# Kernel optimization log

Hardware: AMD Instinct MI355X
Metric: run time of the kernel (lower is better)

The kernel has to match this reference:

```python
import jax, jax.numpy as jnp
import numpy as np

NUM_HEADS = 8

def setup_inputs() -> dict:
    key = jax.random.key(0)
    ks = jax.random.split(key, 12)
    T, B, C, D = 2048, 4, 512, 512
    s = 1.0 / np.sqrt(C)
    return {
        "key_in": jax.random.normal(ks[0], (T, B, C), jnp.float32),
        "value_in": jax.random.normal(ks[1], (T, B, C), jnp.float32),
        "query_in": jax.random.normal(ks[2], (T, B, C), jnp.float32),
        "Wk": jax.random.normal(ks[3], (C, D), jnp.float32) * s,
        "bk": jax.random.normal(ks[4], (D,), jnp.float32) * 0.01,
        "Wv": jax.random.normal(ks[5], (C, D), jnp.float32) * s,
        "bv": jax.random.normal(ks[6], (D,), jnp.float32) * 0.01,
        "Wq": jax.random.normal(ks[7], (C, D), jnp.float32) * s,
        "bq": jax.random.normal(ks[8], (D,), jnp.float32) * 0.01,
        "Wo": jax.random.normal(ks[9], (D, D), jnp.float32) * (1.0 / np.sqrt(D)),
        "bo": jax.random.normal(ks[10], (D,), jnp.float32) * 0.01,
    }

def reference(key_in, value_in, query_in, Wk, bk, Wv, bv, Wq, bq, Wo, bo):
    T, B, C = query_in.shape
    D = Wq.shape[1]
    H = NUM_HEADS
    hd = D // H
    scale = 1.0 / np.sqrt(hd).astype(np.float32)
    # Linear projections on (T, B, C) -> (T, B, D), then the original's
    # row-major view(B, -1, H, hd) followed by transpose(1, 2) -> (B, H, T, hd)
    def proj(x, W, b):
        y = x @ W + b                      # (T, B, D)
        return y.reshape(B, -1, H, hd).transpose(0, 2, 1, 3)  # (B, H, T, hd)
    q = proj(query_in, Wq, bq)
    k = proj(key_in, Wk, bk)
    v = proj(value_in, Wv, bv)
    scores = jnp.einsum("bhqd,bhkd->bhqk", q, k) * scale  # (B, H, T, T)
    attn = jax.nn.softmax(scores, axis=-1)
    x = jnp.einsum("bhqk,bhkd->bhqd", attn, v)            # (B, H, T, hd)
    x = x.transpose(0, 2, 1, 3).reshape(T, B, D)          # matches .view(T, B, d_model)
    return x @ Wo + bo
```

## Files before the change

### kernel.cpp

```cpp
#include <hip/hip_runtime.h>
#include <math.h>

#define MROWS 8192
#define DM    512
#define SEQL  2048
#define HDIM  64
#define NSPLIT 2

typedef __attribute__((ext_vector_type(4))) float floatx4;
typedef _Float16 half2v __attribute__((ext_vector_type(2)));
typedef _Float16 half4v __attribute__((ext_vector_type(4)));
typedef _Float16 half8v __attribute__((ext_vector_type(8)));

#define CEXP 0.18033688011f

__device__ __forceinline__ void gll16(const void* g, void* l) {
    __builtin_amdgcn_global_load_lds(
        (const __attribute__((address_space(1))) unsigned int*)g,
        (__attribute__((address_space(3))) unsigned int*)l, 16, 0, 0);
}

__device__ __forceinline__ half4v pack4(float a, float b, float c, float d) {
    half2v lo = __builtin_bit_cast(half2v, __builtin_amdgcn_cvt_pkrtz(a, b));
    half2v hi = __builtin_bit_cast(half2v, __builtin_amdgcn_cvt_pkrtz(c, d));
    half4v r;
    r[0] = lo[0]; r[1] = lo[1]; r[2] = hi[0]; r[3] = hi[1];
    return r;
}

__global__ __launch_bounds__(256) void transw(const float* __restrict__ w0,
                                              const float* __restrict__ w1,
                                              const float* __restrict__ w2,
                                              const float* __restrict__ w3,
                                              _Float16* __restrict__ t0,
                                              _Float16* __restrict__ t1,
                                              _Float16* __restrict__ t2,
                                              _Float16* __restrict__ t3) {
    __shared__ float tile[32][33];
    const float* W = blockIdx.z == 0 ? w0 : (blockIdx.z == 1 ? w1 : (blockIdx.z == 2 ? w2 : w3));
    _Float16* T = blockIdx.z == 0 ? t0 : (blockIdx.z == 1 ? t1 : (blockIdx.z == 2 ? t2 : t3));
    const float sc = (blockIdx.z == 0) ? CEXP : 1.0f;
    const int tx = threadIdx.x & 31, ty = threadIdx.x >> 5;
    const int x = blockIdx.x * 32 + tx;
    const int y0 = blockIdx.y * 32;
#pragma unroll
    for (int i = 0; i < 4; ++i)
        tile[ty + i * 8][tx] = W[(size_t)(y0 + ty + i * 8) * DM + x];
    __syncthreads();
    const int xo = y0 + tx;
#pragma unroll
    for (int i = 0; i < 4; ++i)
        T[(size_t)(blockIdx.x * 32 + ty + i * 8) * DM + xo] = (_Float16)(tile[tx][ty + i * 8] * sc);
}

__global__ __launch_bounds__(256, 3) void proj_gemm(
        const float* __restrict__ q32, const float* __restrict__ k32, const float* __restrict__ v32,
        const _Float16* __restrict__ Wq, const _Float16* __restrict__ Wk, const _Float16* __restrict__ Wv,
        const float* __restrict__ bq, const float* __restrict__ bk, const float* __restrict__ bv,
        _Float16* __restrict__ Qo, _Float16* __restrict__ Ko, _Float16* __restrict__ Vto) {
    __shared__ _Float16 Bs[512 * 32];
    __shared__ _Float16 As[32 * 32];
    const int z = blockIdx.y;
    const float* A32    = z == 0 ? q32 : (z == 1 ? k32 : v32);
    const _Float16* Bt  = z == 0 ? Wq : (z == 1 ? Wk : Wv);
    const float* bias   = z == 0 ? bq : (z == 1 ? bk : bv);
    const float bscale  = z == 0 ? CEXP : 1.0f;

    const int tid = threadIdx.x;
    const int w = tid >> 6;
    const int l15 = tid & 15, quad = (tid & 63) >> 4;
    const int m0 = blockIdx.x * 32;

    floatx4 acc[2][8];
#pragma unroll
    for (int i = 0; i < 2; ++i)
#pragma unroll
        for (int j = 0; j < 8; ++j) acc[i][j] = (floatx4){0.f, 0.f, 0.f, 0.f};

    for (int kt = 0; kt < DM / 32; ++kt) {
        __syncthreads();
#pragma unroll
        for (int i = 0; i < 8; ++i) {
            const int c = i * 256 + tid;
            const int row = c >> 2, g = c & 3;
            const int kg = g ^ (row & 3);
            gll16(&Bt[(size_t)row * DM + kt * 32 + kg * 8], &Bs[c * 8]);
        }
        if (tid < 128) {
            const int c = tid;
            const int row = c >> 2, g = c & 3;
            const int kg = g ^ (row & 3);
            const float* src = &A32[(size_t)(m0 + row) * DM + kt * 32 + kg * 8];
            const float4 f0 = *(const float4*)&src[0];
            const float4 f1 = *(const float4*)&src[4];
            half8v o;
            o[0] = (_Float16)f0.x; o[1] = (_Float16)f0.y; o[2] = (_Float16)f0.z; o[3] = (_Float16)f0.w;
            o[4] = (_Float16)f1.x; o[5] = (_Float16)f1.y; o[6] = (_Float16)f1.z; o[7] = (_Float16)f1.w;
            *(half8v*)&As[c * 8] = o;
        }
        __syncthreads();
        half8v af[2], bfr[8];
#pragma unroll
        for (int i = 0; i < 2; ++i) {
            const int row = i * 16 + l15;
            af[i] = *(const half8v*)&As[row * 32 + (quad ^ (row & 3)) * 8];
        }
#pragma unroll
        for (int j = 0; j < 8; ++j) {
            const int row = w * 128 + j * 16 + l15;
            bfr[j] = *(const half8v*)&Bs[row * 32 + (quad ^ (row & 3)) * 8];
        }
#pragma unroll
        for (int i = 0; i < 2; ++i)
#pragma unroll
            for (int j = 0; j < 8; ++j)
                acc[i][j] = __builtin_amdgcn_mfma_f32_16x16x32_f16(af[i], bfr[j], acc[i][j], 0, 0, 0);
    }
#pragma unroll
    for (int j = 0; j < 8; ++j) {
        const int col = w * 128 + j * 16 + l15;
        const float bv4 = bias[col] * bscale;
#pragma unroll
        for (int i = 0; i < 2; ++i) {
            const int rb = m0 + i * 16 + quad * 4;
            if (z == 2) {
                const int g = rb >> 11, seq = rb & 2047;
                half4v pv;
#pragma unroll
                for (int r = 0; r < 4; ++r) pv[r] = (_Float16)(acc[i][j][r] + bv4);
                *(half4v*)&Vto[((size_t)g * DM + col) * SEQL + seq] = pv;
            } else {
                _Float16* oh = z == 0 ? Qo : Ko;
#pragma unroll
                for (int r = 0; r < 4; ++r)
                    oh[(size_t)(rb + r) * DM + col] = (_Float16)(acc[i][j][r] + bv4);
            }
        }
    }
}

__global__ __launch_bounds__(256, 4) void out_gemm(
        const _Float16* __restrict__ Op0, const _Float16* __restrict__ Op1,
        const float* __restrict__ lp,
        const _Float16* __restrict__ Wo, const float* __restrict__ bo,
        float* __restrict__ out) {
    __shared__ _Float16 Bs[256 * 64];
    __shared__ _Float16 As[32 * 64];
    const int tid = threadIdx.x;
    const int w = tid >> 6;
    const int l15 = tid & 15, quad = (tid & 63) >> 4;
    const int n0 = blockIdx.x * 256, m0 = blockIdx.y * 32;

    floatx4 acc[2][4];
#pragma unroll
    for (int i = 0; i < 2; ++i)
#pragma unroll
        for (int j = 0; j < 4; ++j) acc[i][j] = (floatx4){0.f, 0.f, 0.f, 0.f};

    for (int kt = 0; kt < DM / 64; ++kt) {
        __syncthreads();
#pragma unroll
        for (int i = 0; i < 8; ++i) {
            const int c = i * 256 + tid;
            const int row = c >> 3, g = c & 7;
            const int kg = g ^ (row & 7);
            gll16(&Wo[(size_t)(n0 + row) * DM + kt * 64 + kg * 8], &Bs[c * 8]);
        }
        {
            const int c = tid;
            const int row = c >> 3, g = c & 7;
            const int kg = g ^ (row & 7);
            const int grow = m0 + row;
            const size_t off = (size_t)grow * DM + kt * 64 + kg * 8;
            const half8v a = *(const half8v*)&Op0[off];
            const half8v b = *(const half8v*)&Op1[off];
            const float inv = 1.0f / (lp[(size_t)grow * 8 + kt] +
                                      lp[((size_t)MROWS + grow) * 8 + kt]);
            half8v s;
#pragma unroll
            for (int e = 0; e < 8; ++e)
                s[e] = (_Float16)(((float)a[e] + (float)b[e]) * inv);
            *(half8v*)&As[c * 8] = s;
        }
        __syncthreads();
#pragma unroll
        for (int ks = 0; ks < 2; ++ks) {
            half8v af[2], bfr[4];
#pragma unroll
            for (int i = 0; i < 2; ++i) {
                const int row = i * 16 + l15;
                af[i] = *(const half8v*)&As[row * 64 + ((ks * 4 + quad) ^ (row & 7)) * 8];
            }
#pragma unroll
            for (int j = 0; j < 4; ++j) {
                const int row = w * 64 + j * 16 + l15;
                bfr[j] = *(const half8v*)&Bs[row * 64 + ((ks * 4 + quad) ^ (row & 7)) * 8];
            }
#pragma unroll
            for (int i = 0; i < 2; ++i)
#pragma unroll
                for (int j = 0; j < 4; ++j)
                    acc[i][j] = __builtin_amdgcn_mfma_f32_16x16x32_f16(af[i], bfr[j], acc[i][j], 0, 0, 0);
        }
    }
#pragma unroll
    for (int j = 0; j < 4; ++j) {
        const int col = n0 + w * 64 + j * 16 + l15;
        const float bv4 = bo[col];
#pragma unroll
        for (int i = 0; i < 2; ++i) {
            const int rb = m0 + i * 16 + quad * 4;
#pragma unroll
            for (int r = 0; r < 4; ++r)
                out[(size_t)(rb + r) * DM + col] = acc[i][j][r] + bv4;
        }
    }
}

__global__ __launch_bounds__(256, 4) void attn_mfma(const _Float16* __restrict__ Q16,
                                                    const _Float16* __restrict__ K16,
                                                    const _Float16* __restrict__ Vt,
                                                    _Float16* __restrict__ Opart,
                                                    float* __restrict__ lpart) {
    __shared__ _Float16 Ks[2][64 * 64];
    __shared__ _Float16 Vs[2][64 * 64];

    const int tid  = threadIdx.x;
    const int lane = tid & 63;
    const int l15  = lane & 15;
    const int quad = lane >> 4;

    const int pair  = blockIdx.y;
    const int split = blockIdx.z;
    const int grp   = pair >> 3;
    const int h     = pair & 7;
    const int q0    = blockIdx.x * 128;
    const int rQ    = grp * SEQL + q0 + (tid >> 6) * 32;
    const int cb    = h * HDIM;
    const int NIT   = (SEQL / 64) / NSPLIT;
    const int kt0   = split * NIT;

    const _Float16* Kbase = K16 + (size_t)grp * SEQL * DM + cb;
    const _Float16* Vbase = Vt + (size_t)grp * DM * SEQL + (size_t)cb * SEQL;

    half8v qf[2][2];
#pragma unroll
    for (int qt = 0; qt < 2; ++qt)
#pragma unroll
        for (int ks = 0; ks < 2; ++ks)
            qf[qt][ks] = *(const half8v*)&Q16[(size_t)(rQ + qt * 16 + l15) * DM + cb + ks * 32 + quad * 8];

    floatx4 oacc[2][4], lacc[2];
#pragma unroll
    for (int qt = 0; qt < 2; ++qt) {
        lacc[qt] = (floatx4){0.f, 0.f, 0.f, 0.f};
#pragma unroll
        for (int dt = 0; dt < 4; ++dt) oacc[qt][dt] = (floatx4){0.f, 0.f, 0.f, 0.f};
    }
    half4v ones;
    ones[0] = (_Float16)1.f; ones[1] = (_Float16)1.f; ones[2] = (_Float16)1.f; ones[3] = (_Float16)1.f;

#define STAGE(KT, B)                                                            \
    {                                                                           \
        _Float16* ksb = &Ks[B][0];                                              \
        _Float16* vsb = &Vs[B][0];                                              \
        _Pragma("unroll")                                                       \
        for (int i_ = 0; i_ < 4; ++i_) {                                        \
            const int c_ = i_ * 256 + tid;                                      \
            if (c_ < 512) {                                                     \
                const int key_ = c_ >> 3, g_ = c_ & 7;                          \
                const int dg_ = g_ ^ (key_ & 7);                                \
                gll16(&Kbase[(size_t)((KT) * 64 + key_) * DM + dg_ * 8],        \
                      &ksb[c_ * 8]);                                            \
            } else {                                                            \
                const int cv_ = c_ - 512;                                       \
                const int d_ = cv_ >> 3, g_ = cv_ & 7;                          \
                const int kg_ = g_ ^ (d_ & 7);                                  \
                gll16(&Vbase[(size_t)d_ * SEQL + (KT) * 64 + kg_ * 8],          \
                      &vsb[cv_ * 8]);                                           \
            }                                                                   \
        }                                                                       \
    }

    STAGE(kt0, 0)

    for (int it = 0; it < NIT; ++it) {
        const int cur = it & 1;
        __syncthreads();
        if (it + 1 < NIT) STAGE(kt0 + it + 1, cur ^ 1)

        const _Float16* ksb = &Ks[cur][0];
        const _Float16* vsb = &Vs[cur][0];

        floatx4 st[4][2];
#pragma unroll
        for (int ktile = 0; ktile < 4; ++ktile) {
            const int key = ktile * 16 + l15;
            const half8v kf0 = *(const half8v*)&ksb[key * 64 + ((0 + quad) ^ (key & 7)) * 8];
            const half8v kf1 = *(const half8v*)&ksb[key * 64 + ((4 + quad) ^ (key & 7)) * 8];
#pragma unroll
            for (int qt = 0; qt < 2; ++qt) {
                floatx4 z = {0.f, 0.f, 0.f, 0.f};
                z = __builtin_amdgcn_mfma_f32_16x16x32_f16(kf0, qf[qt][0], z, 0, 0, 0);
                st[ktile][qt] = __builtin_amdgcn_mfma_f32_16x16x32_f16(kf1, qf[qt][1], z, 0, 0, 0);
            }
        }

        half4v pa[4][2];
#pragma unroll
        for (int ktile = 0; ktile < 4; ++ktile)
#pragma unroll
            for (int qt = 0; qt < 2; ++qt)
                pa[ktile][qt] = pack4(__builtin_amdgcn_exp2f(st[ktile][qt][0]),
                                      __builtin_amdgcn_exp2f(st[ktile][qt][1]),
                                      __builtin_amdgcn_exp2f(st[ktile][qt][2]),
                                      __builtin_amdgcn_exp2f(st[ktile][qt][3]));

#pragma unroll
        for (int qt = 0; qt < 2; ++qt)
#pragma unroll
            for (int ktile = 0; ktile < 4; ++ktile)
                lacc[qt] = __builtin_amdgcn_mfma_f32_16x16x16f16(pa[ktile][qt], ones, lacc[qt], 0, 0, 0);

#pragma unroll
        for (int dt = 0; dt < 4; ++dt) {
            const int d = dt * 16 + l15;
#pragma unroll
            for (int ktile = 0; ktile < 4; ++ktile) {
                const int G = ktile * 2 + (quad >> 1);
                const int slot = G ^ (d & 7);
                const half4v vf = *(const half4v*)&vsb[d * 64 + slot * 8 + (quad & 1) * 4];
#pragma unroll
                for (int qt = 0; qt < 2; ++qt)
                    oacc[qt][dt] = __builtin_amdgcn_mfma_f32_16x16x16f16(pa[ktile][qt], vf, oacc[qt][dt], 0, 0, 0);
            }
        }
    }

    _Float16* Op = Opart + (size_t)split * MROWS * DM;
#pragma unroll
    for (int qt = 0; qt < 2; ++qt)
#pragma unroll
        for (int r = 0; r < 4; ++r) {
            const int qrow = rQ + qt * 16 + quad * 4 + r;
            const size_t rowoff = (size_t)qrow * DM + cb;
#pragma unroll
            for (int dt = 0; dt < 4; ++dt)
                Op[rowoff + dt * 16 + l15] = (_Float16)oacc[qt][dt][r];
            if (l15 == 0)
                lpart[((size_t)split * MROWS + qrow) * 8 + h] = lacc[qt][r];
        }
}

extern "C" void kernel_launch(void* const* d_in, const int* in_sizes, int n_in,
                              void* d_out, int out_size, void* d_ws, size_t ws_size,
                              hipStream_t stream) {
    const float* key_in   = (const float*)d_in[0];
    const float* value_in = (const float*)d_in[1];
    const float* query_in = (const float*)d_in[2];
    const float* Wk = (const float*)d_in[3];
    const float* bk = (const float*)d_in[4];
    const float* Wv = (const float*)d_in[5];
    const float* bv = (const float*)d_in[6];
    const float* Wq = (const float*)d_in[7];
    const float* bq = (const float*)d_in[8];
    const float* Wo = (const float*)d_in[9];
    const float* bo = (const float*)d_in[10];
    float* out = (float*)d_out;

    const size_t MAT = (size_t)MROWS * DM;
    _Float16* Q16  = (_Float16*)d_ws;
    _Float16* K16  = Q16 + MAT;
    _Float16* Vtb  = K16 + MAT;
    _Float16* Wqt  = Vtb + MAT;
    _Float16* Wkt  = Wqt + DM * DM;
    _Float16* Wvt  = Wkt + DM * DM;
    _Float16* Wot  = Wvt + DM * DM;
    float*    lpart = (float*)(Wot + DM * DM);
    _Float16* Opart = (_Float16*)(lpart + 2 * MROWS * 8);

    const dim3 blk(256);

    transw<<<dim3(16, 16, 4), blk, 0, stream>>>(Wq, Wk, Wv, Wo, Wqt, Wkt, Wvt, Wot);

    proj_gemm<<<dim3(MROWS / 32, 3), blk, 0, stream>>>(
        query_in, key_in, value_in, Wqt, Wkt, Wvt, bq, bk, bv, Q16, K16, Vtb);

    attn_mfma<<<dim3(SEQL / 128, 32, NSPLIT), blk, 0, stream>>>(Q16, K16, Vtb, Opart, lpart);

    out_gemm<<<dim3(2, MROWS / 32), blk, 0, stream>>>(
        Opart, Opart + MAT, lpart, Wot, bo, out);
}
```

Measured before the change: 201.6 us.

## Fuse four MHA kernels into one persistent cooperative kernel with grid syncs

The weight transpose, QKV projection, attention and output GEMM are folded into one persistent cooperative kernel. Phases are separated by grid.sync and each block loops over work units, with shared memory reused across phases. This aims to remove per-launch overhead and the gaps between kernels. The output GEMM tile also shrinks to 128 columns, giving more work units. In exchange, grid-wide barriers are added, occupancy is capped at the largest shared-memory footprint of any phase, and blocks may sit idle when a phase's work does not divide evenly across the grid. If the cooperative launch fails, the code falls back to four separate kernel launches.

New measurement: 458.1 us. 2.27x slower.

```diff
diff --git a/kernel.cpp b/kernel.cpp
--- a/kernel.cpp
+++ b/kernel.cpp
@@ -1,5 +1,8 @@
 #include <hip/hip_runtime.h>
+#include <hip/hip_cooperative_groups.h>
 #include <math.h>
+
+namespace cg = cooperative_groups;
 
 #define MROWS 8192
 #define DM    512
@@ -13,6 +16,18 @@
 typedef _Float16 half8v __attribute__((ext_vector_type(8)));
 
 #define CEXP 0.18033688011f
+
+#define SMEM_BYTES 34816
+
+struct MhaArgs {
+    const float *q32, *k32, *v32;
+    const float *Wq32, *Wk32, *Wv32, *Wo32;
+    const float *bq, *bk, *bv, *bo;
+    _Float16 *Wqt, *Wkt, *Wvt, *Wot;
+    _Float16 *Q16, *K16, *Vtb, *Opart;
+    float *lpart;
+    float *out;
+};
 
 __device__ __forceinline__ void gll16(const void* g, void* l) {
     __builtin_amdgcn_global_load_lds(
@@ -28,48 +43,40 @@
     return r;
 }
 
-__global__ __launch_bounds__(256) void transw(const float* __restrict__ w0,
-                                              const float* __restrict__ w1,
-                                              const float* __restrict__ w2,
-                                              const float* __restrict__ w3,
-                                              _Float16* __restrict__ t0,
-                                              _Float16* __restrict__ t1,
-                                              _Float16* __restrict__ t2,
-                                              _Float16* __restrict__ t3) {
-    __shared__ float tile[32][33];
-    const float* W = blockIdx.z == 0 ? w0 : (blockIdx.z == 1 ? w1 : (blockIdx.z == 2 ? w2 : w3));
-    _Float16* T = blockIdx.z == 0 ? t0 : (blockIdx.z == 1 ? t1 : (blockIdx.z == 2 ? t2 : t3));
-    const float sc = (blockIdx.z == 0) ? CEXP : 1.0f;
-    const int tx = threadIdx.x & 31, ty = threadIdx.x >> 5;
-    const int x = blockIdx.x * 32 + tx;
-    const int y0 = blockIdx.y * 32;
+__device__ __forceinline__ void phase0(const MhaArgs& a, int u, int tid,
+                                       unsigned char* smem) {
+    float* tile = (float*)smem;
+    const int z = u >> 8, t = u & 255;
+    const float* W = z == 0 ? a.Wq32 : (z == 1 ? a.Wk32 : (z == 2 ? a.Wv32 : a.Wo32));
+    _Float16* T = z == 0 ? a.Wqt : (z == 1 ? a.Wkt : (z == 2 ? a.Wvt : a.Wot));
+    const float sc = (z == 0) ? CEXP : 1.0f;
+    const int tx = tid & 31, ty = tid >> 5;
+    const int x = (t & 15) * 32 + tx;
+    const int y0 = (t >> 4) * 32;
+    __syncthreads();
 #pragma unroll
     for (int i = 0; i < 4; ++i)
-        tile[ty + i * 8][tx] = W[(size_t)(y0 + ty + i * 8) * DM + x];
+        tile[(ty + i * 8) * 33 + tx] = W[(size_t)(y0 + ty + i * 8) * DM + x];
     __syncthreads();
     const int xo = y0 + tx;
 #pragma unroll
     for (int i = 0; i < 4; ++i)
-        T[(size_t)(blockIdx.x * 32 + ty + i * 8) * DM + xo] = (_Float16)(tile[tx][ty + i * 8] * sc);
-}
-
-__global__ __launch_bounds__(256, 3) void proj_gemm(
-        const float* __restrict__ q32, const float* __restrict__ k32, const float* __restrict__ v32,
-        const _Float16* __restrict__ Wq, const _Float16* __restrict__ Wk, const _Float16* __restrict__ Wv,
-        const float* __restrict__ bq, const float* __restrict__ bk, const float* __restrict__ bv,
-        _Float16* __restrict__ Qo, _Float16* __restrict__ Ko, _Float16* __restrict__ Vto) {
-    __shared__ _Float16 Bs[512 * 32];
-    __shared__ _Float16 As[32 * 32];
-    const int z = blockIdx.y;
-    const float* A32    = z == 0 ? q32 : (z == 1 ? k32 : v32);
-    const _Float16* Bt  = z == 0 ? Wq : (z == 1 ? Wk : Wv);
-    const float* bias   = z == 0 ? bq : (z == 1 ? bk : bv);
-    const float bscale  = z == 0 ? CEXP : 1.0f;
-
-    const int tid = threadIdx.x;
+        T[(size_t)((t & 15) * 32 + ty + i * 8) * DM + xo] =
+            (_Float16)(tile[tx * 33 + ty + i * 8] * sc);
+}
+
+__device__ __forceinline__ void phase1(const MhaArgs& a, int u, int tid,
+                                       unsigned char* smem) {
+    _Float16* Bs = (_Float16*)smem;
+    _Float16* As = (_Float16*)(smem + 32768);
     const int w = tid >> 6;
     const int l15 = tid & 15, quad = (tid & 63) >> 4;
-    const int m0 = blockIdx.x * 32;
+    const int z = u >> 8;
+    const int m0 = (u & 255) * 32;
+    const float* A32   = z == 0 ? a.q32 : (z == 1 ? a.k32 : a.v32);
+    const _Float16* Bt = z == 0 ? a.Wqt : (z == 1 ? a.Wkt : a.Wvt);
+    const float* bias  = z == 0 ? a.bq : (z == 1 ? a.bk : a.bv);
+    const float bscale = z == 0 ? CEXP : 1.0f;
 
     floatx4 acc[2][8];
 #pragma unroll
@@ -128,9 +135,9 @@
                 half4v pv;
 #pragma unroll
                 for (int r = 0; r < 4; ++r) pv[r] = (_Float16)(acc[i][j][r] + bv4);
-                *(half4v*)&Vto[((size_t)g * DM + col) * SEQL + seq] = pv;
+                *(half4v*)&a.Vtb[((size_t)g * DM + col) * SEQL + seq] = pv;
             } else {
-                _Float16* oh = z == 0 ? Qo : Ko;
+                _Float16* oh = z == 0 ? a.Q16 : a.K16;
 #pragma unroll
                 for (int r = 0; r < 4; ++r)
                     oh[(size_t)(rb + r) * DM + col] = (_Float16)(acc[i][j][r] + bv4);
@@ -139,116 +146,33 @@
     }
 }
 
-__global__ __launch_bounds__(256, 4) void out_gemm(
-        const _Float16* __restrict__ Op0, const _Float16* __restrict__ Op1,
-        const float* __restrict__ lp,
-        const _Float16* __restrict__ Wo, const float* __restrict__ bo,
-        float* __restrict__ out) {
-    __shared__ _Float16 Bs[256 * 64];
-    __shared__ _Float16 As[32 * 64];
-    const int tid = threadIdx.x;
+__device__ __forceinline__ void phase2(const MhaArgs& a, int u, int tid,
+                                       unsigned char* smem) {
+    _Float16* KsB = (_Float16*)smem;
+    _Float16* VsB = (_Float16*)(smem + 16384);
     const int w = tid >> 6;
     const int l15 = tid & 15, quad = (tid & 63) >> 4;
-    const int n0 = blockIdx.x * 256, m0 = blockIdx.y * 32;
-
-    floatx4 acc[2][4];
-#pragma unroll
-    for (int i = 0; i < 2; ++i)
-#pragma unroll
-        for (int j = 0; j < 4; ++j) acc[i][j] = (floatx4){0.f, 0.f, 0.f, 0.f};
-
-    for (int kt = 0; kt < DM / 64; ++kt) {
-        __syncthreads();
-#pragma unroll
-        for (int i = 0; i < 8; ++i) {
-            const int c = i * 256 + tid;
-            const int row = c >> 3, g = c & 7;
-            const int kg = g ^ (row & 7);
-            gll16(&Wo[(size_t)(n0 + row) * DM + kt * 64 + kg * 8], &Bs[c * 8]);
-        }
-        {
-            const int c = tid;
-            const int row = c >> 3, g = c & 7;
-            const int kg = g ^ (row & 7);
-            const int grow = m0 + row;
-            const size_t off = (size_t)grow * DM + kt * 64 + kg * 8;
-            const half8v a = *(const half8v*)&Op0[off];
-            const half8v b = *(const half8v*)&Op1[off];
-            const float inv = 1.0f / (lp[(size_t)grow * 8 + kt] +
-                                      lp[((size_t)MROWS + grow) * 8 + kt]);
-            half8v s;
-#pragma unroll
-            for (int e = 0; e < 8; ++e)
-                s[e] = (_Float16)(((float)a[e] + (float)b[e]) * inv);
-            *(half8v*)&As[c * 8] = s;
-        }
-        __syncthreads();
-#pragma unroll
-        for (int ks = 0; ks < 2; ++ks) {
-            half8v af[2], bfr[4];
-#pragma unroll
-            for (int i = 0; i < 2; ++i) {
-                const int row = i * 16 + l15;
-                af[i] = *(const half8v*)&As[row * 64 + ((ks * 4 + quad) ^ (row & 7)) * 8];
-            }
-#pragma unroll
-            for (int j = 0; j < 4; ++j) {
-                const int row = w * 64 + j * 16 + l15;
-                bfr[j] = *(const half8v*)&Bs[row * 64 + ((ks * 4 + quad) ^ (row & 7)) * 8];
-            }
-#pragma unroll
-            for (int i = 0; i < 2; ++i)
-#pragma unroll
-                for (int j = 0; j < 4; ++j)
-                    acc[i][j] = __builtin_amdgcn_mfma_f32_16x16x32_f16(af[i], bfr[j], acc[i][j], 0, 0, 0);
-        }
-    }
-#pragma unroll
-    for (int j = 0; j < 4; ++j) {
-        const int col = n0 + w * 64 + j * 16 + l15;
-        const float bv4 = bo[col];
-#pragma unroll
-        for (int i = 0; i < 2; ++i) {
-            const int rb = m0 + i * 16 + quad * 4;
-#pragma unroll
-            for (int r = 0; r < 4; ++r)
-                out[(size_t)(rb + r) * DM + col] = acc[i][j][r] + bv4;
-        }
-    }
-}
-
-__global__ __launch_bounds__(256, 4) void attn_mfma(const _Float16* __restrict__ Q16,
-                                                    const _Float16* __restrict__ K16,
-                                                    const _Float16* __restrict__ Vt,
-                                                    _Float16* __restrict__ Opart,
-                                                    float* __restrict__ lpart) {
-    __shared__ _Float16 Ks[2][64 * 64];
-    __shared__ _Float16 Vs[2][64 * 64];
-
-    const int tid  = threadIdx.x;
-    const int lane = tid & 63;
-    const int l15  = lane & 15;
-    const int quad = lane >> 4;
-
-    const int pair  = blockIdx.y;
-    const int split = blockIdx.z;
+
+    const int qtile = u & 15;
+    const int pair  = (u >> 4) & 31;
+    const int split = u >> 9;
     const int grp   = pair >> 3;
     const int h     = pair & 7;
-    const int q0    = blockIdx.x * 128;
-    const int rQ    = grp * SEQL + q0 + (tid >> 6) * 32;
+    const int q0    = qtile * 128;
+    const int rQ    = grp * SEQL + q0 + w * 32;
     const int cb    = h * HDIM;
     const int NIT   = (SEQL / 64) / NSPLIT;
     const int kt0   = split * NIT;
 
-    const _Float16* Kbase = K16 + (size_t)grp * SEQL * DM + cb;
-    const _Float16* Vbase = Vt + (size_t)grp * DM * SEQL + (size_t)cb * SEQL;
+    const _Float16* Kbase = a.K16 + (size_t)grp * SEQL * DM + cb;
+    const _Float16* Vbase = a.Vtb + (size_t)grp * DM * SEQL + (size_t)cb * SEQL;
 
     half8v qf[2][2];
 #pragma unroll
     for (int qt = 0; qt < 2; ++qt)
 #pragma unroll
         for (int ks = 0; ks < 2; ++ks)
-            qf[qt][ks] = *(const half8v*)&Q16[(size_t)(rQ + qt * 16 + l15) * DM + cb + ks * 32 + quad * 8];
+            qf[qt][ks] = *(const half8v*)&a.Q16[(size_t)(rQ + qt * 16 + l15) * DM + cb + ks * 32 + quad * 8];
 
     floatx4 oacc[2][4], lacc[2];
 #pragma unroll
@@ -262,8 +186,8 @@
 
 #define STAGE(KT, B)                                                            \
     {                                                                           \
-        _Float16* ksb = &Ks[B][0];                                              \
-        _Float16* vsb = &Vs[B][0];                                              \
+        _Float16* ksb = &KsB[(B) * 4096];                                       \
+        _Float16* vsb = &VsB[(B) * 4096];                                       \
         _Pragma("unroll")                                                       \
         for (int i_ = 0; i_ < 4; ++i_) {                                        \
             const int c_ = i_ * 256 + tid;                                      \
@@ -289,8 +213,8 @@
         __syncthreads();
         if (it + 1 < NIT) STAGE(kt0 + it + 1, cur ^ 1)
 
-        const _Float16* ksb = &Ks[cur][0];
-        const _Float16* vsb = &Vs[cur][0];
+        const _Float16* ksb = &KsB[cur * 4096];
+        const _Float16* vsb = &VsB[cur * 4096];
 
         floatx4 st[4][2];
 #pragma unroll
@@ -300,9 +224,9 @@
             const half8v kf1 = *(const half8v*)&ksb[key * 64 + ((4 + quad) ^ (key & 7)) * 8];
 #pragma unroll
             for (int qt = 0; qt < 2; ++qt) {
-                floatx4 z = {0.f, 0.f, 0.f, 0.f};
-                z = __builtin_amdgcn_mfma_f32_16x16x32_f16(kf0, qf[qt][0], z, 0, 0, 0);
-                st[ktile][qt] = __builtin_amdgcn_mfma_f32_16x16x32_f16(kf1, qf[qt][1], z, 0, 0, 0);
+                floatx4 z2 = {0.f, 0.f, 0.f, 0.f};
+                z2 = __builtin_amdgcn_mfma_f32_16x16x32_f16(kf0, qf[qt][0], z2, 0, 0, 0);
+                st[ktile][qt] = __builtin_amdgcn_mfma_f32_16x16x32_f16(kf1, qf[qt][1], z2, 0, 0, 0);
             }
         }
 
@@ -336,8 +260,9 @@
             }
         }
     }
-
-    _Float16* Op = Opart + (size_t)split * MROWS * DM;
+#undef STAGE
+
+    _Float16* Op = a.Opart + (size_t)split * MROWS * DM;
 #pragma unroll
     for (int qt = 0; qt < 2; ++qt)
 #pragma unroll
@@ -348,46 +273,159 @@
             for (int dt = 0; dt < 4; ++dt)
                 Op[rowoff + dt * 16 + l15] = (_Float16)oacc[qt][dt][r];
             if (l15 == 0)
-                lpart[((size_t)split * MROWS + qrow) * 8 + h] = lacc[qt][r];
-        }
+                a.lpart[((size_t)split * MROWS + qrow) * 8 + h] = lacc[qt][r];
+        }
+}
+
+__device__ __forceinline__ void phase3(const MhaArgs& a, int u, int tid,
+                                       unsigned char* smem) {
+    _Float16* Bs = (_Float16*)smem;
+    _Float16* As = (_Float16*)(smem + 16384);
+    const int w = tid >> 6;
+    const int l15 = tid & 15, quad = (tid & 63) >> 4;
+    const int n0 = (u & 3) * 128;
+    const int m0 = (u >> 2) * 32;
+
+    floatx4 acc[2][2];
+#pragma unroll
+    for (int i = 0; i < 2; ++i)
+#pragma unroll
+        for (int j = 0; j < 2; ++j) acc[i][j] = (floatx4){0.f, 0.f, 0.f, 0.f};
+
+    for (int kt = 0; kt < DM / 64; ++kt) {
+        __syncthreads();
+#pragma unroll
+        for (int i = 0; i < 4; ++i) {
+            const int c = i * 256 + tid;
+            const int row = c >> 3, g = c & 7;
+            const int kg = g ^ (row & 7);
+            gll16(&a.Wot[(size_t)(n0 + row) * DM + kt * 64 + kg * 8], &Bs[c * 8]);
+        }
+        {
+            const int c = tid;
+            const int row = c >> 3, g = c & 7;
+            const int kg = g ^ (row & 7);
+            const int grow = m0 + row;
+            const size_t off = (size_t)grow * DM + kt * 64 + kg * 8;
+            const half8v av = *(const half8v*)&a.Opart[off];
+            const half8v bv = *(const half8v*)&a.Opart[(size_t)MROWS * DM + off];
+            const float inv = 1.0f / (a.lpart[(size_t)grow * 8 + kt] +
+                                      a.lpart[((size_t)MROWS + grow) * 8 + kt]);
+            half8v s;
+#pragma unroll
+            for (int e = 0; e < 8; ++e)
+                s[e] = (_Float16)(((float)av[e] + (float)bv[e]) * inv);
+            *(half8v*)&As[c * 8] = s;
+        }
+        __syncthreads();
+#pragma unroll
+        for (int ks = 0; ks < 2; ++ks) {
+            half8v af[2], bfr[2];
+#pragma unroll
+            for (int i = 0; i < 2; ++i) {
+                const int row = i * 16 + l15;
+                af[i] = *(const half8v*)&As[row * 64 + ((ks * 4 + quad) ^ (row & 7)) * 8];
+            }
+#pragma unroll
+            for (int j = 0; j < 2; ++j) {
+                const int row = w * 32 + j * 16 + l15;
+                bfr[j] = *(const half8v*)&Bs[row * 64 + ((ks * 4 + quad) ^ (row & 7)) * 8];
+            }
+#pragma unroll
+            for (int i = 0; i < 2; ++i)
+#pragma unroll
+                for (int j = 0; j < 2; ++j)
+                    acc[i][j] = __builtin_amdgcn_mfma_f32_16x16x32_f16(af[i], bfr[j], acc[i][j], 0, 0, 0);
+        }
+    }
+#pragma unroll
+    for (int j = 0; j < 2; ++j) {
+        const int col = n0 + w * 32 + j * 16 + l15;
+        const float bv4 = a.bo[col];
+#pragma unroll
+        for (int i = 0; i < 2; ++i) {
+            const int rb = m0 + i * 16 + quad * 4;
+#pragma unroll
+            for (int r = 0; r < 4; ++r)
+                a.out[(size_t)(rb + r) * DM + col] = acc[i][j][r] + bv4;
+        }
+    }
+}
+
+__global__ __launch_bounds__(256, 4) void fused_mha(MhaArgs a) {
+    __shared__ __align__(16) unsigned char smem[SMEM_BYTES];
+    cg::grid_group grid = cg::this_grid();
+    const int tid = threadIdx.x;
+    for (unsigned u = blockIdx.x; u < 1024; u += gridDim.x) phase0(a, u, tid, smem);
+    grid.sync();
+    for (unsigned u = blockIdx.x; u < 768; u += gridDim.x) phase1(a, u, tid, smem);
+    grid.sync();
+    for (unsigned u = blockIdx.x; u < 1024; u += gridDim.x) phase2(a, u, tid, smem);
+    grid.sync();
+    for (unsigned u = blockIdx.x; u < 1024; u += gridDim.x) phase3(a, u, tid, smem);
+}
+
+__global__ __launch_bounds__(256, 4) void k_p0(MhaArgs a) {
+    __shared__ __align__(16) unsigned char smem[SMEM_BYTES];
+    phase0(a, blockIdx.x, threadIdx.x, smem);
+}
+__global__ __launch_bounds__(256, 4) void k_p1(MhaArgs a) {
+    __shared__ __align__(16) unsigned char smem[SMEM_BYTES];
+    phase1(a, blockIdx.x, threadIdx.x, smem);
+}
+__global__ __launch_bounds__(256, 4) void k_p2(MhaArgs a) {
+    __shared__ __align__(16) unsigned char smem[SMEM_BYTES];
+    phase2(a, blockIdx.x, threadIdx.x, smem);
+}
+__global__ __launch_bounds__(256, 4) void k_p3(MhaArgs a) {
+    __shared__ __align__(16) unsigned char smem[SMEM_BYTES];
+    phase3(a, blockIdx.x, threadIdx.x, smem);
 }
 
 extern "C" void kernel_launch(void* const* d_in, const int* in_sizes, int n_in,
                               void* d_out, int out_size, void* d_ws, size_t ws_size,
                               hipStream_t stream) {
-    const float* key_in   = (const float*)d_in[0];
-    const float* value_in = (const float*)d_in[1];
-    const float* query_in = (const float*)d_in[2];
-    const float* Wk = (const float*)d_in[3];
-    const float* bk = (const float*)d_in[4];
-    const float* Wv = (const float*)d_in[5];
-    const float* bv = (const float*)d_in[6];
-    const float* Wq = (const float*)d_in[7];
-    const float* bq = (const float*)d_in[8];
-    const float* Wo = (const float*)d_in[9];
-    const float* bo = (const float*)d_in[10];
-    float* out = (float*)d_out;
+    MhaArgs a;
+    a.k32  = (const float*)d_in[0];
+    a.v32  = (const float*)d_in[1];
+    a.q32  = (const float*)d_in[2];
+    a.Wk32 = (const float*)d_in[3];
+    a.bk   = (const float*)d_in[4];
+    a.Wv32 = (const float*)d_in[5];
+    a.bv   = (const float*)d_in[6];
+    a.Wq32 = (const float*)d_in[7];
+    a.bq   = (const float*)d_in[8];
+    a.Wo32 = (const float*)d_in[9];
+    a.bo   = (const float*)d_in[10];
+    a.out  = (float*)d_out;
 
     const size_t MAT = (size_t)MROWS * DM;
-    _Float16* Q16  = (_Float16*)d_ws;
-    _Float16* K16  = Q16 + MAT;
-    _Float16* Vtb  = K16 + MAT;
-    _Float16* Wqt  = Vtb + MAT;
-    _Float16* Wkt  = Wqt + DM * DM;
-    _Float16* Wvt  = Wkt + DM * DM;
-    _Float16* Wot  = Wvt + DM * DM;
-    float*    lpart = (float*)(Wot + DM * DM);
-    _Float16* Opart = (_Float16*)(lpart + 2 * MROWS * 8);
-
-    const dim3 blk(256);
-
-    transw<<<dim3(16, 16, 4), blk, 0, stream>>>(Wq, Wk, Wv, Wo, Wqt, Wkt, Wvt, Wot);
-
-    proj_gemm<<<dim3(MROWS / 32, 3), blk, 0, stream>>>(
-        query_in, key_in, value_in, Wqt, Wkt, Wvt, bq, bk, bv, Q16, K16, Vtb);
-
-    attn_mfma<<<dim3(SEQL / 128, 32, NSPLIT), blk, 0, stream>>>(Q16, K16, Vtb, Opart, lpart);
-
-    out_gemm<<<dim3(2, MROWS / 32), blk, 0, stream>>>(
-        Opart, Opart + MAT, lpart, Wot, bo, out);
-}
+    a.Q16  = (_Float16*)d_ws;
+    a.K16  = a.Q16 + MAT;
+    a.Vtb  = a.K16 + MAT;
+    a.Wqt  = a.Vtb + MAT;
+    a.Wkt  = a.Wqt + DM * DM;
+    a.Wvt  = a.Wkt + DM * DM;
+    a.Wot  = a.Wvt + DM * DM;
+    a.lpart = (float*)(a.Wot + DM * DM);
+    a.Opart = (_Float16*)(a.lpart + 2 * MROWS * 8);
+
+    int maxAct = 0;
+    hipError_t e = hipOccupancyMaxActiveBlocksPerMultiprocessor(
+        &maxAct, (const void*)fused_mha, 256, 0);
+    bool coop_ok = (e == hipSuccess) && (maxAct >= 1);
+    if (coop_ok) {
+        int grid = maxAct * 256;
+        if (grid > 1024) grid = 1024;
+        void* args[] = {(void*)&a};
+        e = hipLaunchCooperativeKernel((const void*)fused_mha, dim3(grid),
+                                       dim3(256), args, 0, stream);
+        coop_ok = (e == hipSuccess);
+    }
+    if (!coop_ok) {
+        k_p0<<<dim3(1024), dim3(256), 0, stream>>>(a);
+        k_p1<<<dim3(768),  dim3(256), 0, stream>>>(a);
+        k_p2<<<dim3(1024), dim3(256), 0, stream>>>(a);
+        k_p3<<<dim3(1024), dim3(256), 0, stream>>>(a);
+    }
+}
```
